# Performance work log

Hardware: AMD Instinct MI355X
Metric: run time of the kernel (lower is better)

## Reference

```python
import jax, jax.numpy as jnp
import numpy as np

UNITS = 512
M = 8
INPUT_DIM = 512
BATCH = 2048


def setup_inputs() -> dict:
    key = jax.random.key(0)
    ks = jax.random.split(key, 9)
    D, U = INPUT_DIM, UNITS
    fused_dim = D + U
    def glorot(k, shape):
        lim = np.sqrt(6.0 / (shape[0] + shape[1])).astype(np.float32)
        return jax.random.uniform(k, shape, jnp.float32, -lim, lim)
    return {
        "inputs": jax.random.normal(ks[0], (BATCH, D), jnp.float32),
        "elapsed": jax.random.uniform(ks[1], (BATCH, 1), jnp.float32),
        "state": jax.random.normal(ks[2], (BATCH, U * M), jnp.float32),
        "W_r": glorot(ks[3], (fused_dim, U * M)),
        "b_r": jnp.zeros((U * M,), jnp.float32),
        "W_d": glorot(ks[4], (fused_dim, U)),
        "b_d": jnp.zeros((U,), jnp.float32),
        "W_u": glorot(ks[5], (fused_dim, U * M)),
        "b_u": jnp.zeros((U * M,), jnp.float32),
    }


def reference(inputs, elapsed, state, W_r, b_r, W_d, b_d, W_u, b_u):
    B = inputs.shape[0]
    # tau_i = 10**(i/2)  =>  ln_tau_i = i * 0.5 * ln(10)
    ln_tau_table = 0.5 * jnp.log(jnp.float32(10.0)) * jnp.arange(M, dtype=jnp.float32)  # [M]
    tau_table = jnp.exp(ln_tau_table)  # [M]

    h_hat = state.reshape(B, UNITS, M)            # [B, U, M]
    h = h_hat.sum(axis=2)                          # [B, U]
    fused = jnp.concatenate([inputs, h], axis=-1)  # [B, D+U]

    # retrieval gate: softmax over M buckets of -(ln_tau_r - table)^2
    ln_tau_r = (fused @ W_r + b_r).reshape(B, UNITS, M)
    rki = jax.nn.softmax(-jnp.square(ln_tau_r - ln_tau_table), axis=2)
    q_input = jnp.sum(rki * h_hat, axis=2)         # [B, U]

    # detect (candidate) with tanh
    reset_value = jnp.concatenate([inputs, q_input], axis=1)
    qk = jnp.tanh(reset_value @ W_d + b_d)[:, :, None]  # [B, U, 1]

    # update gate
    ln_tau_s = (fused @ W_u + b_u).reshape(B, UNITS, M)
    ski = jax.nn.softmax(-jnp.square(ln_tau_s - ln_tau_table), axis=2)

    # exponential decay per bucket: elapsed [B,1] / tau [M] -> [B, M]
    exp_term = jnp.exp(-elapsed / tau_table)[:, None, :]  # [B, 1, M]
    h_hat_next = ((1.0 - ski) * h_hat + ski * qk) * exp_term  # [B, U, M]

    h_next = h_hat_next.sum(axis=2)                # [B, U]
    return h_next, h_hat_next.reshape(B, UNITS * M)
```

## Files before the change

### kernel.cpp

```cpp
#include <hip/hip_runtime.h>
#include <hip/hip_fp16.h>
#include <cmath>

#define B_SZ 2048
#define D_IN 512
#define U_N  512
#define FD   1024
#define NRU  4096
#define NRU2 8192

typedef _Float16 f16x8 __attribute__((ext_vector_type(8)));
typedef float    f32x4 __attribute__((ext_vector_type(4)));

typedef const __attribute__((address_space(1))) void glb_cv;
typedef __attribute__((address_space(3))) void lds_v;

#define TAB_INIT {0.0f, 1.15129254649702f, 2.30258509299405f, \
                  3.45387763949107f, 4.60517018598809f, 5.75646273248511f, \
                  6.90775527898214f, 8.05904782547916f}

__global__ __launch_bounds__(256) void prep_kernel(
    const float* __restrict__ inputs, const float* __restrict__ state,
    __half* __restrict__ fused, __half* __restrict__ reset)
{
    const int b = blockIdx.x;
    const int t = threadIdx.x;

    const float2 iv = *(const float2*)(inputs + (size_t)b * D_IN + t * 2);
    __half2 hv;
    hv.x = __float2half(iv.x);
    hv.y = __float2half(iv.y);
    *(__half2*)(fused + (size_t)b * FD + t * 2) = hv;
    *(__half2*)(reset + (size_t)b * FD + t * 2) = hv;

    const float4* sp = (const float4*)(state + (size_t)b * NRU + t * 16);
    float4 x0 = sp[0], x1 = sp[1], x2 = sp[2], x3 = sp[3];
    float s0 = (x0.x + x0.y) + (x0.z + x0.w) + (x1.x + x1.y) + (x1.z + x1.w);
    float s1 = (x2.x + x2.y) + (x2.z + x2.w) + (x3.x + x3.y) + (x3.z + x3.w);
    __half2 h2;
    h2.x = __float2half(s0);
    h2.y = __float2half(s1);
    *(__half2*)(fused + (size_t)b * FD + D_IN + t * 2) = h2;
}

__global__ __launch_bounds__(256) void convT3_kernel(
    const float* __restrict__ W_r, const float* __restrict__ W_u,
    const float* __restrict__ W_d, __half* __restrict__ WruT,
    __half* __restrict__ WdT)
{
    __shared__ float tile[32][33];
    const int bx = blockIdx.x;
    const float* W;
    __half* Wt;
    int N, nt;
    if (bx < 128)      { W = W_r; Wt = WruT;                    N = NRU; nt = bx * 32; }
    else if (bx < 256) { W = W_u; Wt = WruT + (size_t)NRU * FD; N = NRU; nt = (bx - 128) * 32; }
    else               { W = W_d; Wt = WdT;                     N = U_N; nt = (bx - 256) * 32; }

    const int kt = blockIdx.y * 32;
    const int t  = threadIdx.x;
    const int c  = t & 31;
    const int r4 = t >> 5;

#pragma unroll
    for (int i = 0; i < 4; i++) {
        int r = r4 + i * 8;
        tile[r][c] = W[(size_t)(kt + r) * N + nt + c];
    }
    __syncthreads();
#pragma unroll
    for (int i = 0; i < 4; i++) {
        int rr = r4 + i * 8;
        Wt[(size_t)(nt + rr) * FD + kt + c] = __float2half(tile[c][rr]);
    }
}

template <int BM, int EPI>
__global__ __launch_bounds__(256) void gemm_k(
    const __half* __restrict__ A, const __half* __restrict__ Bt,
    const float* __restrict__ biasA, const float* __restrict__ biasB, int nsplit,
    float* __restrict__ C, int Ncols,
    const float* __restrict__ state, __half* __restrict__ resetw,
    __half* __restrict__ skibuf, int K)
{
    extern __shared__ __align__(16) char smem[];
    __half* sA = (__half*)smem;
    __half* sB = (__half*)(smem + BM * 128);

    const int t    = threadIdx.x;
    const int m0   = blockIdx.y * BM;
    const int n0   = blockIdx.x << 7;
    const int lane = t & 63;
    const int w    = t >> 6;
    const int m16  = lane & 15;
    const int quad = lane >> 4;
    constexpr int MI = BM / 32;
    constexpr int IA = BM / 32;
    const int wm = (w & 1) * (BM / 2);
    const int wn = (w >> 1) << 6;
    const int strip = w >> 1;

    f32x4 acc[MI][4];
#pragma unroll
    for (int i = 0; i < MI; i++)
#pragma unroll
        for (int j = 0; j < 4; j++)
#pragma unroll
            for (int r = 0; r < 4; r++) acc[i][j][r] = 0.f;

    const __half* gAp[IA];
    const __half* lAp[IA];
#pragma unroll
    for (int i = 0; i < IA; i++) {
        const int off = w * (BM * 32) + i * 1024 + lane * 16;
        const int row = off >> 7;
        const int g   = ((off & 127) >> 4) ^ (row & 7);
        gAp[i] = A + (size_t)(m0 + row) * K + g * 8;
        lAp[i] = sA + ((w * (BM * 32) + i * 1024) >> 1);
    }
    const __half* gBp[4];
    const __half* lBp[4];
#pragma unroll
    for (int i = 0; i < 4; i++) {
        const int off = w * 4096 + i * 1024 + lane * 16;
        const int row = off >> 7;
        const int g   = ((off & 127) >> 4) ^ (row & 7);
        gBp[i] = Bt + (size_t)(n0 + row) * K + g * 8;
        lBp[i] = sB + ((w * 4096 + i * 1024) >> 1);
    }

    for (int kt = 0; kt < K; kt += 64) {
        __syncthreads();
#pragma unroll
        for (int i = 0; i < IA; i++)
            __builtin_amdgcn_global_load_lds((glb_cv*)(gAp[i] + kt), (lds_v*)lAp[i], 16, 0, 0);
#pragma unroll
        for (int i = 0; i < 4; i++)
            __builtin_amdgcn_global_load_lds((glb_cv*)(gBp[i] + kt), (lds_v*)lBp[i], 16, 0, 0);
        __syncthreads();

#pragma unroll
        for (int s = 0; s < 2; s++) {
            f16x8 af[MI], bf[4];
#pragma unroll
            for (int mi = 0; mi < MI; mi++) {
                const int row = wm + mi * 16 + m16;
                const int gi  = (s * 4 + quad) ^ (row & 7);
                af[mi] = *(const f16x8*)(sA + row * 64 + gi * 8);
            }
#pragma unroll
            for (int ni = 0; ni < 4; ni++) {
                const int row = wn + ni * 16 + m16;
                const int gi  = (s * 4 + quad) ^ (row & 7);
                bf[ni] = *(const f16x8*)(sB + row * 64 + gi * 8);
            }
#pragma unroll
            for (int mi = 0; mi < MI; mi++)
#pragma unroll
                for (int ni = 0; ni < 4; ni++)
                    acc[mi][ni] = __builtin_amdgcn_mfma_f32_16x16x32_f16(
                        af[mi], bf[ni], acc[mi][ni], 0, 0, 0);
        }
    }

    if constexpr (EPI == 0) {
#pragma unroll
        for (int mi = 0; mi < MI; mi++) {
#pragma unroll
            for (int ni = 0; ni < 4; ni++) {
                const int col = n0 + wn + ni * 16 + m16;
                const float bv = biasA[col];
#pragma unroll
                for (int r = 0; r < 4; r++) {
                    const int row = m0 + wm + mi * 16 + quad * 4 + r;
                    C[(size_t)row * Ncols + col] = tanhf(acc[mi][ni][r] + bv);
                }
            }
        }
    } else {
        __syncthreads();
        float*  ebuf = (float*)smem;
        __half* qbuf = (__half*)(smem + 128 * 36 * 4);
        const bool is_r = (n0 < nsplit);
        const float* bp = is_r ? biasA : biasB;
        const int n0r = is_r ? n0 : n0 - nsplit;
        const float TAB[8] = TAB_INIT;
        const int ug  = t & 3;
        const int s   = ug >> 1;
        const int g   = ug & 1;
        const int bl0 = t >> 2;

        for (int ni = 0; ni < 4; ni++) {
            const float bv = bp[n0r + strip * 64 + ni * 16 + m16];
#pragma unroll
            for (int mi = 0; mi < 4; mi++)
#pragma unroll
                for (int r = 0; r < 4; r++)
                    ebuf[(wm + mi * 16 + quad * 4 + r) * 36 + strip * 16 + m16] =
                        acc[mi][ni][r] + bv;
            __syncthreads();

#pragma unroll
            for (int p = 0; p < 2; p++) {
                const int b_loc = bl0 + p * 64;
                const int b = m0 + b_loc;
                const float* rowp = ebuf + b_loc * 36 + ug * 8;
                float v[8];
                *(float4*)&v[0] = *(const float4*)rowp;
                *(float4*)&v[4] = *(const float4*)(rowp + 4);

                float e[8];
                float sum = 0.f;
#pragma unroll
                for (int i = 0; i < 8; i++) {
                    float d = v[i] - TAB[i];
                    e[i] = __expf(-d * d);
                    sum += e[i];
                }
                const int col = n0r + s * 64 + ni * 16 + g * 8;
                if (is_r) {
                    const float4 h0 = *(const float4*)(state + (size_t)b * NRU + col);
                    const float4 h1 = *(const float4*)(state + (size_t)b * NRU + col + 4);
                    const float hv[8] = {h0.x, h0.y, h0.z, h0.w, h1.x, h1.y, h1.z, h1.w};
                    float qn = 0.f;
#pragma unroll
                    for (int i = 0; i < 8; i++) qn += e[i] * hv[i];
                    qbuf[b_loc * 16 + (s * 8 + ni * 2 + g)] = __float2half(qn / sum);
                } else {
                    const float inv = 1.0f / sum;
                    __half2 o[4];
#pragma unroll
                    for (int i = 0; i < 4; i++) {
                        o[i].x = __float2half(e[2 * i] * inv);
                        o[i].y = __float2half(e[2 * i + 1] * inv);
                    }
                    *(uint4*)(skibuf + (size_t)b * NRU + col) = *(uint4*)o;
                }
            }
            __syncthreads();
        }
        if (is_r) {
            const int b_loc = t >> 1;
            const int j = t & 1;
            uint4 qv = *(uint4*)(qbuf + b_loc * 16 + j * 8);
            *(uint4*)(resetw + (size_t)(m0 + b_loc) * FD + D_IN + (n0r >> 3) + j * 8) = qv;
        }
    }
}

__global__ __launch_bounds__(256) void final_kernel(
    const __half* __restrict__ skibuf, const float* __restrict__ state,
    const float* __restrict__ qk, const float* __restrict__ elapsed,
    float* __restrict__ out0, float* __restrict__ out1)
{
    const int idx = blockIdx.x * 256 + threadIdx.x;
    const int b = idx >> 9;
    const int u = idx & 511;

    const float INV_TAU[8] = {1.0f, 0.316227766016838f, 0.1f, 0.0316227766016838f,
                              0.01f, 0.00316227766016838f, 0.001f, 0.000316227766016838f};

    const uint4 sr = *(const uint4*)(skibuf + (size_t)b * NRU + u * 8);
    const __half2* sh = (const __half2*)&sr;
    float sk[8];
#pragma unroll
    for (int i = 0; i < 4; i++) {
        float2 f2 = __half22float2(sh[i]);
        sk[2 * i]     = f2.x;
        sk[2 * i + 1] = f2.y;
    }

    const float4* hh = (const float4*)(state + ((size_t)b * NRU + u * 8));
    float4 h0 = hh[0], h1 = hh[1];
    float h[8] = {h0.x, h0.y, h0.z, h0.w, h1.x, h1.y, h1.z, h1.w};

    const float q  = qk[(size_t)b * U_N + u];
    const float el = elapsed[b];

    float hn[8];
    float acc = 0.f;
#pragma unroll
    for (int i = 0; i < 8; i++) {
        const float et = __expf(-el * INV_TAU[i]);
        hn[i] = ((1.0f - sk[i]) * h[i] + sk[i] * q) * et;
        acc += hn[i];
    }

    float4* o = (float4*)(out1 + ((size_t)b * NRU + u * 8));
    o[0] = make_float4(hn[0], hn[1], hn[2], hn[3]);
    o[1] = make_float4(hn[4], hn[5], hn[6], hn[7]);
    out0[(size_t)b * U_N + u] = acc;
}

extern "C" void kernel_launch(void* const* d_in, const int* in_sizes, int n_in,
                              void* d_out, int out_size, void* d_ws, size_t ws_size,
                              hipStream_t stream)
{
    (void)in_sizes; (void)n_in; (void)out_size; (void)ws_size;

    const float* inputs  = (const float*)d_in[0];
    const float* elapsed = (const float*)d_in[1];
    const float* state   = (const float*)d_in[2];
    const float* W_r     = (const float*)d_in[3];
    const float* b_r     = (const float*)d_in[4];
    const float* W_d     = (const float*)d_in[5];
    const float* b_d     = (const float*)d_in[6];
    const float* W_u     = (const float*)d_in[7];
    const float* b_u     = (const float*)d_in[8];
    float* out = (float*)d_out;

    char* ws = (char*)d_ws;
    __half* fused  = (__half*)(ws);
    __half* reset  = (__half*)(ws + ((size_t)4  << 20));
    __half* WruT   = (__half*)(ws + ((size_t)8  << 20));
    __half* WdT    = (__half*)(ws + ((size_t)24 << 20));
    __half* skibuf = (__half*)(ws + ((size_t)25 << 20));
    float*  qk     = (float*) (ws + ((size_t)41 << 20));

    prep_kernel<<<B_SZ, 256, 0, stream>>>(inputs, state, fused, reset);
    convT3_kernel<<<dim3(272, FD / 32), 256, 0, stream>>>(W_r, W_u, W_d, WruT, WdT);

    gemm_k<128, 1><<<dim3(NRU2 / 128, B_SZ / 128), 256, 32768, stream>>>(
        fused, WruT, b_r, b_u, NRU, nullptr, 0, state, reset, skibuf, FD);

    gemm_k<64, 0><<<dim3(U_N / 128, B_SZ / 64), 256, 24576, stream>>>(
        reset, WdT, b_d, nullptr, 1 << 30, qk, U_N, nullptr, nullptr, nullptr, FD);

    final_kernel<<<(B_SZ * U_N) / 256, 256, 0, stream>>>(skibuf, state, qk, elapsed, out,
                                                         out + (size_t)B_SZ * U_N);
}
```

Measured before the change: 212.3 us.

## Double-buffer GEMM LDS tiles with register prefetch of the next K slice

Replaces the single-buffered direct global-to-LDS loads (64-wide K tiles, two syncs per tile) with a ping-pong LDS scheme over 32-wide K slices. Each step loads the next slice into registers, runs the MFMAs on the current buffer, then stores to the other buffer, so there is one barrier per step. The goal is to hide global load latency behind MFMA work. The cost is more register pressure, a redundant final prefetch, and twice as many smaller iterations. The epilogue's LDS usage may also need to fit the new buffer sizing.

```diff
diff --git a/kernel.cpp b/kernel.cpp
--- a/kernel.cpp
+++ b/kernel.cpp
@@ -11,9 +11,6 @@
 
 typedef _Float16 f16x8 __attribute__((ext_vector_type(8)));
 typedef float    f32x4 __attribute__((ext_vector_type(4)));
-
-typedef const __attribute__((address_space(1))) void glb_cv;
-typedef __attribute__((address_space(3))) void lds_v;
 
 #define TAB_INIT {0.0f, 1.15129254649702f, 2.30258509299405f, \
                   3.45387763949107f, 4.60517018598809f, 5.75646273248511f, \
@@ -84,8 +81,9 @@
     __half* __restrict__ skibuf, int K)
 {
     extern __shared__ __align__(16) char smem[];
-    __half* sA = (__half*)smem;
-    __half* sB = (__half*)(smem + BM * 128);
+    constexpr int TILEH = (BM + 128) * 32;
+    __half* s0 = (__half*)smem;
+    __half* s1 = s0 + TILEH;
 
     const int t    = threadIdx.x;
     const int m0   = blockIdx.y * BM;
@@ -95,7 +93,7 @@
     const int m16  = lane & 15;
     const int quad = lane >> 4;
     constexpr int MI = BM / 32;
-    constexpr int IA = BM / 32;
+    constexpr int GA = BM / 64;
     const int wm = (w & 1) * (BM / 2);
     const int wn = (w >> 1) << 6;
     const int strip = w >> 1;
@@ -108,59 +106,78 @@
 #pragma unroll
             for (int r = 0; r < 4; r++) acc[i][j][r] = 0.f;
 
-    const __half* gAp[IA];
-    const __half* lAp[IA];
-#pragma unroll
-    for (int i = 0; i < IA; i++) {
-        const int off = w * (BM * 32) + i * 1024 + lane * 16;
-        const int row = off >> 7;
-        const int g   = ((off & 127) >> 4) ^ (row & 7);
-        gAp[i] = A + (size_t)(m0 + row) * K + g * 8;
-        lAp[i] = sA + ((w * (BM * 32) + i * 1024) >> 1);
-    }
-    const __half* gBp[4];
-    const __half* lBp[4];
-#pragma unroll
-    for (int i = 0; i < 4; i++) {
-        const int off = w * 4096 + i * 1024 + lane * 16;
-        const int row = off >> 7;
-        const int g   = ((off & 127) >> 4) ^ (row & 7);
-        gBp[i] = Bt + (size_t)(n0 + row) * K + g * 8;
-        lBp[i] = sB + ((w * 4096 + i * 1024) >> 1);
-    }
-
-    for (int kt = 0; kt < K; kt += 64) {
+    const __half* gA[GA];
+    int lA[GA];
+#pragma unroll
+    for (int i = 0; i < GA; i++) {
+        const int off = t * 16 + i * 4096;
+        const int row = off >> 6;
+        const int g   = (off >> 4) & 3;
+        gA[i] = A + (size_t)(m0 + row) * K + g * 8;
+        lA[i] = row * 32 + ((g ^ ((row >> 1) & 3)) << 3);
+    }
+    const __half* gB[2];
+    int lB[2];
+#pragma unroll
+    for (int i = 0; i < 2; i++) {
+        const int off = t * 16 + i * 4096;
+        const int row = off >> 6;
+        const int g   = (off >> 4) & 3;
+        gB[i] = Bt + (size_t)(n0 + row) * K + g * 8;
+        lB[i] = BM * 32 + row * 32 + ((g ^ ((row >> 1) & 3)) << 3);
+    }
+
+    {
+        uint4 ra[GA], rb[2];
+#pragma unroll
+        for (int i = 0; i < GA; i++) ra[i] = *(const uint4*)(gA[i]);
+#pragma unroll
+        for (int i = 0; i < 2; i++)  rb[i] = *(const uint4*)(gB[i]);
+#pragma unroll
+        for (int i = 0; i < GA; i++) *(uint4*)(s0 + lA[i]) = ra[i];
+#pragma unroll
+        for (int i = 0; i < 2; i++)  *(uint4*)(s0 + lB[i]) = rb[i];
+    }
+    __syncthreads();
+
+    auto step = [&](const __half* curb, __half* nxtb, int konext) {
+        uint4 ra[GA], rb[2];
+#pragma unroll
+        for (int i = 0; i < GA; i++) ra[i] = *(const uint4*)(gA[i] + konext);
+#pragma unroll
+        for (int i = 0; i < 2; i++)  rb[i] = *(const uint4*)(gB[i] + konext);
+
+        f16x8 af[MI], bf[4];
+#pragma unroll
+        for (int mi = 0; mi < MI; mi++) {
+            const int row = wm + mi * 16 + m16;
+            af[mi] = *(const f16x8*)(curb + row * 32 + ((quad ^ ((row >> 1) & 3)) << 3));
+        }
+#pragma unroll
+        for (int ni = 0; ni < 4; ni++) {
+            const int row = wn + ni * 16 + m16;
+            bf[ni] = *(const f16x8*)(curb + BM * 32 + row * 32 + ((quad ^ ((row >> 1) & 3)) << 3));
+        }
+#pragma unroll
+        for (int mi = 0; mi < MI; mi++)
+#pragma unroll
+            for (int ni = 0; ni < 4; ni++)
+                acc[mi][ni] = __builtin_amdgcn_mfma_f32_16x16x32_f16(
+                    af[mi], bf[ni], acc[mi][ni], 0, 0, 0);
+
+#pragma unroll
+        for (int i = 0; i < GA; i++) *(uint4*)(nxtb + lA[i]) = ra[i];
+#pragma unroll
+        for (int i = 0; i < 2; i++)  *(uint4*)(nxtb + lB[i]) = rb[i];
         __syncthreads();
-#pragma unroll
-        for (int i = 0; i < IA; i++)
-            __builtin_amdgcn_global_load_lds((glb_cv*)(gAp[i] + kt), (lds_v*)lAp[i], 16, 0, 0);
-#pragma unroll
-        for (int i = 0; i < 4; i++)
-            __builtin_amdgcn_global_load_lds((glb_cv*)(gBp[i] + kt), (lds_v*)lBp[i], 16, 0, 0);
-        __syncthreads();
-
-#pragma unroll
-        for (int s = 0; s < 2; s++) {
-            f16x8 af[MI], bf[4];
-#pragma unroll
-            for (int mi = 0; mi < MI; mi++) {
-                const int row = wm + mi * 16 + m16;
-                const int gi  = (s * 4 + quad) ^ (row & 7);
-                af[mi] = *(const f16x8*)(sA + row * 64 + gi * 8);
-            }
-#pragma unroll
-            for (int ni = 0; ni < 4; ni++) {
-                const int row = wn + ni * 16 + m16;
-                const int gi  = (s * 4 + quad) ^ (row & 7);
-                bf[ni] = *(const f16x8*)(sB + row * 64 + gi * 8);
-            }
-#pragma unroll
-            for (int mi = 0; mi < MI; mi++)
-#pragma unroll
-                for (int ni = 0; ni < 4; ni++)
-                    acc[mi][ni] = __builtin_amdgcn_mfma_f32_16x16x32_f16(
-                        af[mi], bf[ni], acc[mi][ni], 0, 0, 0);
-        }
+    };
+
+    const int NI = K >> 5;
+    for (int k = 0; k < NI; k += 2) {
+        const int k1 = k + 1;
+        const int k2 = (k + 2 < NI) ? k + 2 : NI - 1;
+        step(s0, s1, k1 << 5);
+        step(s1, s0, k2 << 5);
     }
 
     if constexpr (EPI == 0) {
```

Result: slower. 219.1 us (+3.2%).
